# Kernel optimization log

Hardware: AMD Instinct MI355X
Metric: run time of the kernel (lower is better)

The kernel has to match this reference:

```python
import jax, jax.numpy as jnp
import numpy as np

B, H, E_DIM, V = 512, 2048, 1024, 50257


def setup_inputs() -> dict:
    key = jax.random.key(0)
    ks = jax.random.split(key, 10)
    s_e = 1.0 / np.sqrt(E_DIM)
    s_h = 1.0 / np.sqrt(H)
    return {
        "inp": jax.random.randint(ks[0], (B,), 0, V),
        "h_0": jax.random.normal(ks[1], (B, H), jnp.float32) * 0.1,
        "c_0": jax.random.normal(ks[2], (B, H), jnp.float32) * 0.1,
        "E": jax.random.normal(ks[3], (V, E_DIM), jnp.float32),
        "Wx": jax.random.normal(ks[4], (4, H, E_DIM), jnp.float32) * s_e,
        "bx": jax.random.normal(ks[5], (4, H), jnp.float32) * s_e,
        "Wh": jax.random.normal(ks[6], (4, H, H), jnp.float32) * s_h,
        "bh": jax.random.normal(ks[7], (4, H), jnp.float32) * s_h,
        "Wd": jax.random.normal(ks[8], (V, H), jnp.float32) * s_h,
        "bd": jax.random.normal(ks[9], (V,), jnp.float32) * s_h,
    }


def reference(inp, h_0, c_0, E, Wx, bx, Wh, bh, Wd, bd):
    # Embedding lookup: [B, E_DIM]
    x = E[inp]
    # Two fused GEMMs for all 4 gates (gate order: f, i, o, c): [B, 4, H]
    gates = (jnp.einsum('be,ghe->bgh', x, Wx) + bx[None]
             + jnp.einsum('bh,gkh->bgk', h_0, Wh) + bh[None])
    f_g = jax.nn.sigmoid(gates[:, 0])
    i_g = jax.nn.sigmoid(gates[:, 1])
    o_g = jax.nn.sigmoid(gates[:, 2])
    c_tilda = jnp.tanh(gates[:, 3])
    cx = f_g * c_0 + i_g * c_tilda
    hx = o_g * jnp.tanh(cx)
    out = hx @ Wd.T + bd  # [B, V]
    return out, hx, cx
```

## Files before the change

### kernel.cpp

```cpp
#include <hip/hip_runtime.h>
#include <hip/hip_bf16.h>

using bf16x8 = __attribute__((ext_vector_type(8))) short;
using f32x4  = __attribute__((ext_vector_type(4))) float;

#define DEVI __device__ __forceinline__

DEVI unsigned short bf16r(float f)
{
    return __builtin_bit_cast(unsigned short, __float2bfloat16(f));
}

DEVI bf16x8 cvt8(const f32x4 a, const f32x4 b)
{
    bf16x8 r;
#pragma unroll
    for (int j = 0; j < 4; ++j) {
        r[j]     = (short)bf16r(a[j]);
        r[4 + j] = (short)bf16r(b[j]);
    }
    return r;
}

__global__ __launch_bounds__(256) void k_gather(const float* __restrict__ E,
                                                const int* __restrict__ inp,
                                                unsigned short* __restrict__ x)
{
    const int b = blockIdx.x;
    const long r = inp[b];
    const f32x4 v = ((const f32x4*)(E + r * 1024L))[threadIdx.x];
    ushort4 o;
    o.x = bf16r(v[0]); o.y = bf16r(v[1]); o.z = bf16r(v[2]); o.w = bf16r(v[3]);
    ((ushort4*)(x + (long)b * 1024L))[threadIdx.x] = o;
}

__global__ __launch_bounds__(256) void k_cvtn(const float* __restrict__ in,
                                              unsigned short* __restrict__ out)
{
    const long i = (blockIdx.x * 256L + threadIdx.x) * 8;
    const f32x4 a = *(const f32x4*)(in + i);
    const f32x4 b = *(const f32x4*)(in + i + 4);
    *(bf16x8*)(out + i) = cvt8(a, b);
}


DEVI void mfma_tile512(const char* sA, const char* sB, int l, int wr, int wc,
                       f32x4 (&acc)[8][4])
{
    const int j = l >> 4;
    bf16x8 af[8], bq[4];
#pragma unroll
    for (int m = 0; m < 8; ++m) {
        const int row = wr * 128 + m * 16 + (l & 15);
        af[m] = *(const bf16x8*)(sA + row * 64 + ((j ^ (row & 3)) << 4));
    }
#pragma unroll
    for (int n = 0; n < 4; ++n) {
        const int row = wc * 64 + n * 16 + (l & 15);
        bq[n] = *(const bf16x8*)(sB + row * 64 + ((j ^ (row & 3)) << 4));
    }
#pragma unroll
    for (int m = 0; m < 8; ++m)
#pragma unroll
        for (int n = 0; n < 4; ++n)
            acc[m][n] = __builtin_amdgcn_mfma_f32_16x16x32_bf16(
                af[m], bq[n], acc[m][n], 0, 0, 0);
}

template <bool CLAMP>
DEVI void gemm_core512(const unsigned short* __restrict__ A, long lda,
                       const float* __restrict__ B, long ldb, long bcol0,
                       long bmax, int nt, long kbase, int t, char* lds,
                       f32x4 (&acc)[8][4])
{
    char* sA0 = lds;
    char* sA1 = lds + 32768;
    char* sB0 = lds + 65536;
    char* sB1 = lds + 73728;
    const int l = t & 63, w = t >> 6, wr = w >> 1, wc = w & 1;

    const unsigned short* ap[4];
    int aswz[4];
#pragma unroll
    for (int i = 0; i < 4; ++i) {
        const int g = i * 512 + t, row = g >> 2, j = g & 3;
        ap[i] = A + row * lda + kbase + j * 8;
        aswz[i] = row * 64 + ((j ^ (row & 3)) << 4);
    }
    const int brow = t >> 2, bseg = t & 3;
    long br = bcol0 + brow;
    if (CLAMP) br = (br < bmax) ? br : (bmax - 1);
    const float* bp = B + br * ldb + kbase + bseg * 8;
    const int bswz = brow * 64 + ((bseg ^ (brow & 3)) << 4);

    bf16x8 ra0[4], ra1[4];
    f32x4 rb0[2], rb1[2];

#define LOADR(as, bs)                                                          \
    do {                                                                       \
        _Pragma("unroll") for (int i = 0; i < 4; ++i) {                        \
            as[i] = *(const bf16x8*)ap[i];                                     \
            ap[i] += 32;                                                       \
        }                                                                      \
        bs[0] = *(const f32x4*)bp;                                             \
        bs[1] = *(const f32x4*)(bp + 4);                                       \
        bp += 32;                                                              \
    } while (0)
#define WRLDS(sa, sb, as, bs)                                                  \
    do {                                                                       \
        _Pragma("unroll") for (int i = 0; i < 4; ++i)                          \
            *(bf16x8*)((sa) + aswz[i]) = as[i];                                \
        *(bf16x8*)((sb) + bswz) = cvt8(bs[0], bs[1]);                          \
    } while (0)
#define WAITV6  asm volatile("s_waitcnt vmcnt(6)" ::: "memory")
#define WAITV0  asm volatile("s_waitcnt vmcnt(0)" ::: "memory")
#define WAITL0  asm volatile("s_waitcnt lgkmcnt(0)" ::: "memory")
#define BARRIER __builtin_amdgcn_s_barrier()

    LOADR(ra0, rb0);
    LOADR(ra1, rb1);
    WAITV6;
    WRLDS(sA0, sB0, ra0, rb0);
    LOADR(ra0, rb0);
    WAITL0; BARRIER;

    for (int kt = 0; kt < nt; kt += 2) {
        if (kt + 2 < nt) WAITV6; else WAITV0;
        WRLDS(sA1, sB1, ra1, rb1);
        if (kt + 3 < nt) LOADR(ra1, rb1);
        mfma_tile512(sA0, sB0, l, wr, wc, acc);
        WAITL0; BARRIER;
        if (kt + 2 < nt) {
            if (kt + 3 < nt) WAITV6; else WAITV0;
            WRLDS(sA0, sB0, ra0, rb0);
            if (kt + 4 < nt) LOADR(ra0, rb0);
        }
        mfma_tile512(sA1, sB1, l, wr, wc, acc);
        WAITL0; BARRIER;
    }
#undef LOADR
#undef WRLDS
#undef WAITV6
#undef WAITV0
#undef WAITL0
#undef BARRIER
}

__global__ __launch_bounds__(512) void k_gates(
    const unsigned short* __restrict__ xb, const float* __restrict__ Wx,
    const unsigned short* __restrict__ h0b, const float* __restrict__ Wh,
    float* __restrict__ g0, float* __restrict__ g1, float* __restrict__ g2)
{
    extern __shared__ __align__(16) char lds[];
    const int t = threadIdx.x;
    const int bid = blockIdx.x;
    const int z = bid >> 6;
    const int ntile = bid & 63;

    const unsigned short* A; const float* B; long lda, ldb, kbase; float* C;
    if (z == 0)      { A = xb;  lda = 1024; B = Wx; ldb = 1024; kbase = 0;    C = g0; }
    else if (z == 1) { A = h0b; lda = 2048; B = Wh; ldb = 2048; kbase = 0;    C = g1; }
    else             { A = h0b; lda = 2048; B = Wh; ldb = 2048; kbase = 1024; C = g2; }

    f32x4 acc[8][4] = {};
    gemm_core512<false>(A, lda, B, ldb, (long)ntile * 128, 1L << 40, 32, kbase,
                        t, lds, acc);

    const int l = t & 63, w = t >> 6, wr = w >> 1, wc = w & 1;
    const int lc = l & 15, r4 = (l >> 4) * 4;
#pragma unroll
    for (int n = 0; n < 4; ++n) {
        const long col = (long)ntile * 128 + wc * 64 + n * 16 + lc;
#pragma unroll
        for (int m = 0; m < 8; ++m) {
            const long row = wr * 128 + m * 16 + r4;
#pragma unroll
            for (int r = 0; r < 4; ++r)
                C[(row + r) * 8192 + col] = acc[m][n][r];
        }
    }
}

__global__ __launch_bounds__(512) void k_dec(
    const unsigned short* __restrict__ hxb, const float* __restrict__ Wd,
    const float* __restrict__ bd, float* __restrict__ out)
{
    extern __shared__ __align__(16) char lds[];
    const int t = threadIdx.x;
    const int ntile = blockIdx.x;
    const long N = 50257;

    f32x4 acc[8][4] = {};
    gemm_core512<true>(hxb, 2048, Wd, 2048, (long)ntile * 128, N, 64, 0,
                       t, lds, acc);

    const int l = t & 63, w = t >> 6, wr = w >> 1, wc = w & 1;
    const int lc = l & 15, r4 = (l >> 4) * 4;
#pragma unroll
    for (int n = 0; n < 4; ++n) {
        const long col = (long)ntile * 128 + wc * 64 + n * 16 + lc;
        if (col >= N) continue;
        const float bias = bd[col];
#pragma unroll
        for (int m = 0; m < 8; ++m) {
            const long row = wr * 128 + m * 16 + r4;
#pragma unroll
            for (int r = 0; r < 4; ++r)
                out[(row + r) * N + col] = acc[m][n][r] + bias;
        }
    }
}

__global__ __launch_bounds__(256) void k_lstm(
    const float* __restrict__ g0, const float* __restrict__ g1,
    const float* __restrict__ g2, const float* __restrict__ bx,
    const float* __restrict__ bh, const float* __restrict__ c0,
    float* __restrict__ hx, float* __restrict__ cx,
    unsigned short* __restrict__ hxb)
{
    const int i = blockIdx.x * 256 + threadIdx.x;
    const int b = i >> 9;
    const int hc = (i & 511) << 2;
    const long base = (long)b * 8192;

    f32x4 g[4];
#pragma unroll
    for (int gi = 0; gi < 4; ++gi) {
        const long off = base + gi * 2048 + hc;
        const int boff = gi * 2048 + hc;
        g[gi] = *(const f32x4*)(g0 + off);
        g[gi] += *(const f32x4*)(g1 + off);
        g[gi] += *(const f32x4*)(g2 + off);
        g[gi] += *(const f32x4*)(bx + boff);
        g[gi] += *(const f32x4*)(bh + boff);
    }
    const f32x4 c0v = *(const f32x4*)(c0 + (long)b * 2048 + hc);

    f32x4 cv, hv;
    ushort4 hb;
#pragma unroll
    for (int j = 0; j < 4; ++j) {
        const float fg = 1.f / (1.f + __expf(-g[0][j]));
        const float ig = 1.f / (1.f + __expf(-g[1][j]));
        const float og = 1.f / (1.f + __expf(-g[2][j]));
        const float e2 = __expf(2.f * g[3][j]);
        const float ct = 1.f - 2.f / (e2 + 1.f);
        const float c  = fg * c0v[j] + ig * ct;
        const float e2c = __expf(2.f * c);
        const float th  = 1.f - 2.f / (e2c + 1.f);
        cv[j] = c;
        hv[j] = og * th;
    }
    hb.x = bf16r(hv[0]); hb.y = bf16r(hv[1]); hb.z = bf16r(hv[2]); hb.w = bf16r(hv[3]);

    const long o = (long)b * 2048 + hc;
    *(f32x4*)(cx + o) = cv;
    *(f32x4*)(hx + o) = hv;
    *(ushort4*)(hxb + o) = hb;
}

extern "C" void kernel_launch(void* const* d_in, const int* in_sizes, int n_in,
                              void* d_out, int out_size, void* d_ws, size_t ws_size,
                              hipStream_t stream)
{
    const int*   inp = (const int*)d_in[0];
    const float* h0  = (const float*)d_in[1];
    const float* c0  = (const float*)d_in[2];
    const float* E   = (const float*)d_in[3];
    const float* Wx  = (const float*)d_in[4];
    const float* bx  = (const float*)d_in[5];
    const float* Wh  = (const float*)d_in[6];
    const float* bh  = (const float*)d_in[7];
    const float* Wd  = (const float*)d_in[8];
    const float* bd  = (const float*)d_in[9];

    float* out = (float*)d_out;
    float* hx  = out + 512L * 50257L;
    float* cx  = hx + 512L * 2048L;

    unsigned short* xb  = (unsigned short*)out;
    float* g0 = out + (1L << 20);
    float* g1 = out + (5L << 20);
    float* g2 = out + (9L << 20);
    unsigned short* h0b = (unsigned short*)(out + (13L << 20));
    unsigned short* hxb = (unsigned short*)d_ws;

    k_gather<<<512, 256, 0, stream>>>(E, inp, xb);
    k_cvtn<<<512, 256, 0, stream>>>(h0, h0b);

    k_gates<<<192, 512, 81920, stream>>>(xb, Wx, h0b, Wh, g0, g1, g2);

    k_lstm<<<1024, 256, 0, stream>>>(g0, g1, g2, bx, bh, c0, hx, cx, hxb);

    k_dec<<<393, 512, 81920, stream>>>(hxb, Wd, bd, out);
}
```

Measured before the change: 290.8 us.

## Use 1024-thread blocks with 64-wide K tiles, single LDS buffer, XCD-aware block mapping

The GEMM core now runs 16 waves per block with a 4x4 MFMA tile per wave, loads 64-wide K slices with an 8-way XOR swizzle, and swaps LDS double buffering for a single buffer with extra barriers. Block IDs are remapped so that consecutive tiles land on the same XCD, which should improve L2 reuse of the shared A operand. The decoder grid is padded to 400 blocks and the surplus blocks exit early. Dropping double buffering adds barrier stalls between the MFMA phase and the LDS writes, while doubling the wave count is meant to hide that latency.

New measurement: 806.6 us. +177.4%, slower.

```diff
diff --git a/kernel.cpp b/kernel.cpp
--- a/kernel.cpp
+++ b/kernel.cpp
@@ -44,54 +44,55 @@
 }
 
 
-DEVI void mfma_tile512(const char* sA, const char* sB, int l, int wr, int wc,
-                       f32x4 (&acc)[8][4])
-{
-    const int j = l >> 4;
-    bf16x8 af[8], bq[4];
-#pragma unroll
-    for (int m = 0; m < 8; ++m) {
-        const int row = wr * 128 + m * 16 + (l & 15);
-        af[m] = *(const bf16x8*)(sA + row * 64 + ((j ^ (row & 3)) << 4));
-    }
-#pragma unroll
-    for (int n = 0; n < 4; ++n) {
-        const int row = wc * 64 + n * 16 + (l & 15);
-        bq[n] = *(const bf16x8*)(sB + row * 64 + ((j ^ (row & 3)) << 4));
-    }
-#pragma unroll
-    for (int m = 0; m < 8; ++m)
+DEVI bf16x8 lds_frag(const char* lds, int row, int j)
+{
+    return *(const bf16x8*)(lds + row * 128 + ((j ^ (row & 7)) << 4));
+}
+
+DEVI void mfma_tile16(const char* sA, const char* sB, int l, int wr, int wc,
+                      f32x4 (&acc)[4][4])
+{
+#pragma unroll
+    for (int ks = 0; ks < 2; ++ks) {
+        bf16x8 af[4], bq[4];
+#pragma unroll
+        for (int m = 0; m < 4; ++m)
+            af[m] = lds_frag(sA, wr * 64 + m * 16 + (l & 15), ks * 4 + (l >> 4));
 #pragma unroll
         for (int n = 0; n < 4; ++n)
-            acc[m][n] = __builtin_amdgcn_mfma_f32_16x16x32_bf16(
-                af[m], bq[n], acc[m][n], 0, 0, 0);
+            bq[n] = lds_frag(sB, wc * 64 + n * 16 + (l & 15), ks * 4 + (l >> 4));
+#pragma unroll
+        for (int m = 0; m < 4; ++m)
+#pragma unroll
+            for (int n = 0; n < 4; ++n)
+                acc[m][n] = __builtin_amdgcn_mfma_f32_16x16x32_bf16(
+                    af[m], bq[n], acc[m][n], 0, 0, 0);
+    }
 }
 
 template <bool CLAMP>
-DEVI void gemm_core512(const unsigned short* __restrict__ A, long lda,
-                       const float* __restrict__ B, long ldb, long bcol0,
-                       long bmax, int nt, long kbase, int t, char* lds,
-                       f32x4 (&acc)[8][4])
-{
-    char* sA0 = lds;
-    char* sA1 = lds + 32768;
-    char* sB0 = lds + 65536;
-    char* sB1 = lds + 73728;
+DEVI void gemm_core16(const unsigned short* __restrict__ A, long lda,
+                      const float* __restrict__ B, long ldb, long brow0,
+                      long bmax, int nt, long kbase, int t, char* lds,
+                      f32x4 (&acc)[4][4])
+{
+    char* sA = lds;
+    char* sB = lds + 65536;
     const int l = t & 63, w = t >> 6, wr = w >> 1, wc = w & 1;
 
     const unsigned short* ap[4];
     int aswz[4];
 #pragma unroll
     for (int i = 0; i < 4; ++i) {
-        const int g = i * 512 + t, row = g >> 2, j = g & 3;
+        const int g = i * 1024 + t, row = g >> 3, j = g & 7;
         ap[i] = A + row * lda + kbase + j * 8;
-        aswz[i] = row * 64 + ((j ^ (row & 3)) << 4);
-    }
-    const int brow = t >> 2, bseg = t & 3;
-    long br = bcol0 + brow;
+        aswz[i] = row * 128 + ((j ^ (row & 7)) << 4);
+    }
+    const int brow = t >> 3, bj = t & 7;
+    long br = brow0 + brow;
     if (CLAMP) br = (br < bmax) ? br : (bmax - 1);
-    const float* bp = B + br * ldb + kbase + bseg * 8;
-    const int bswz = brow * 64 + ((bseg ^ (brow & 3)) << 4);
+    const float* bp = B + br * ldb + kbase + bj * 8;
+    const int bswz = brow * 128 + ((bj ^ (brow & 7)) << 4);
 
     bf16x8 ra0[4], ra1[4];
     f32x4 rb0[2], rb1[2];
@@ -100,17 +101,17 @@
     do {                                                                       \
         _Pragma("unroll") for (int i = 0; i < 4; ++i) {                        \
             as[i] = *(const bf16x8*)ap[i];                                     \
-            ap[i] += 32;                                                       \
+            ap[i] += 64;                                                       \
         }                                                                      \
         bs[0] = *(const f32x4*)bp;                                             \
         bs[1] = *(const f32x4*)(bp + 4);                                       \
-        bp += 32;                                                              \
+        bp += 64;                                                              \
     } while (0)
-#define WRLDS(sa, sb, as, bs)                                                  \
+#define WRLDS(as, bs)                                                          \
     do {                                                                       \
         _Pragma("unroll") for (int i = 0; i < 4; ++i)                          \
-            *(bf16x8*)((sa) + aswz[i]) = as[i];                                \
-        *(bf16x8*)((sb) + bswz) = cvt8(bs[0], bs[1]);                          \
+            *(bf16x8*)(sA + aswz[i]) = as[i];                                  \
+        *(bf16x8*)(sB + bswz) = cvt8(bs[0], bs[1]);                            \
     } while (0)
 #define WAITV6  asm volatile("s_waitcnt vmcnt(6)" ::: "memory")
 #define WAITV0  asm volatile("s_waitcnt vmcnt(0)" ::: "memory")
@@ -120,23 +121,25 @@
     LOADR(ra0, rb0);
     LOADR(ra1, rb1);
     WAITV6;
-    WRLDS(sA0, sB0, ra0, rb0);
+    WRLDS(ra0, rb0);
     LOADR(ra0, rb0);
     WAITL0; BARRIER;
 
     for (int kt = 0; kt < nt; kt += 2) {
+        mfma_tile16(sA, sB, l, wr, wc, acc);
+        BARRIER;
         if (kt + 2 < nt) WAITV6; else WAITV0;
-        WRLDS(sA1, sB1, ra1, rb1);
+        WRLDS(ra1, rb1);
         if (kt + 3 < nt) LOADR(ra1, rb1);
-        mfma_tile512(sA0, sB0, l, wr, wc, acc);
         WAITL0; BARRIER;
+        mfma_tile16(sA, sB, l, wr, wc, acc);
+        BARRIER;
         if (kt + 2 < nt) {
             if (kt + 3 < nt) WAITV6; else WAITV0;
-            WRLDS(sA0, sB0, ra0, rb0);
+            WRLDS(ra0, rb0);
             if (kt + 4 < nt) LOADR(ra0, rb0);
+            WAITL0; BARRIER;
         }
-        mfma_tile512(sA1, sB1, l, wr, wc, acc);
-        WAITL0; BARRIER;
     }
 #undef LOADR
 #undef WRLDS
@@ -146,7 +149,7 @@
 #undef BARRIER
 }
 
-__global__ __launch_bounds__(512) void k_gates(
+__global__ __launch_bounds__(1024) void k_gates(
     const unsigned short* __restrict__ xb, const float* __restrict__ Wx,
     const unsigned short* __restrict__ h0b, const float* __restrict__ Wh,
     float* __restrict__ g0, float* __restrict__ g1, float* __restrict__ g2)
@@ -154,17 +157,19 @@
     extern __shared__ __align__(16) char lds[];
     const int t = threadIdx.x;
     const int bid = blockIdx.x;
-    const int z = bid >> 6;
-    const int ntile = bid & 63;
+    const int xcd = bid & 7, slot = bid >> 3;
+    const int L = xcd * 24 + slot;
+    const int z = L >> 6;
+    const int ntile = L & 63;
 
     const unsigned short* A; const float* B; long lda, ldb, kbase; float* C;
     if (z == 0)      { A = xb;  lda = 1024; B = Wx; ldb = 1024; kbase = 0;    C = g0; }
     else if (z == 1) { A = h0b; lda = 2048; B = Wh; ldb = 2048; kbase = 0;    C = g1; }
     else             { A = h0b; lda = 2048; B = Wh; ldb = 2048; kbase = 1024; C = g2; }
 
-    f32x4 acc[8][4] = {};
-    gemm_core512<false>(A, lda, B, ldb, (long)ntile * 128, 1L << 40, 32, kbase,
-                        t, lds, acc);
+    f32x4 acc[4][4] = {};
+    gemm_core16<false>(A, lda, B, ldb, (long)ntile * 128, 1L << 40, 16, kbase,
+                       t, lds, acc);
 
     const int l = t & 63, w = t >> 6, wr = w >> 1, wc = w & 1;
     const int lc = l & 15, r4 = (l >> 4) * 4;
@@ -172,8 +177,8 @@
     for (int n = 0; n < 4; ++n) {
         const long col = (long)ntile * 128 + wc * 64 + n * 16 + lc;
 #pragma unroll
-        for (int m = 0; m < 8; ++m) {
-            const long row = wr * 128 + m * 16 + r4;
+        for (int m = 0; m < 4; ++m) {
+            const long row = wr * 64 + m * 16 + r4;
 #pragma unroll
             for (int r = 0; r < 4; ++r)
                 C[(row + r) * 8192 + col] = acc[m][n][r];
@@ -181,18 +186,22 @@
     }
 }
 
-__global__ __launch_bounds__(512) void k_dec(
+__global__ __launch_bounds__(1024) void k_dec(
     const unsigned short* __restrict__ hxb, const float* __restrict__ Wd,
     const float* __restrict__ bd, float* __restrict__ out)
 {
     extern __shared__ __align__(16) char lds[];
     const int t = threadIdx.x;
-    const int ntile = blockIdx.x;
+    const int bid = blockIdx.x;
+    const int xcd = bid & 7, slot = bid >> 3;
+    const int L = xcd * 50 + slot;
+    if (L >= 393) return;
+    const int ntile = L;
     const long N = 50257;
 
-    f32x4 acc[8][4] = {};
-    gemm_core512<true>(hxb, 2048, Wd, 2048, (long)ntile * 128, N, 64, 0,
-                       t, lds, acc);
+    f32x4 acc[4][4] = {};
+    gemm_core16<true>(hxb, 2048, Wd, 2048, (long)ntile * 128, N, 32, 0,
+                      t, lds, acc);
 
     const int l = t & 63, w = t >> 6, wr = w >> 1, wc = w & 1;
     const int lc = l & 15, r4 = (l >> 4) * 4;
@@ -202,8 +211,8 @@
         if (col >= N) continue;
         const float bias = bd[col];
 #pragma unroll
-        for (int m = 0; m < 8; ++m) {
-            const long row = wr * 128 + m * 16 + r4;
+        for (int m = 0; m < 4; ++m) {
+            const long row = wr * 64 + m * 16 + r4;
 #pragma unroll
             for (int r = 0; r < 4; ++r)
                 out[(row + r) * N + col] = acc[m][n][r] + bias;
@@ -288,9 +297,9 @@
     k_gather<<<512, 256, 0, stream>>>(E, inp, xb);
     k_cvtn<<<512, 256, 0, stream>>>(h0, h0b);
 
-    k_gates<<<192, 512, 81920, stream>>>(xb, Wx, h0b, Wh, g0, g1, g2);
+    k_gates<<<192, 1024, 81920, stream>>>(xb, Wx, h0b, Wh, g0, g1, g2);
 
     k_lstm<<<1024, 256, 0, stream>>>(g0, g1, g2, bx, bh, c0, hx, cx, hxb);
 
-    k_dec<<<393, 512, 81920, stream>>>(hxb, Wd, bd, out);
-}
+    k_dec<<<400, 1024, 81920, stream>>>(hxb, Wd, bd, out);
+}
```
